# Performance work log

Measured on AMD Instinct MI355X. Metric: run time of the kernel, lower is better.

## Reference

```python
import jax, jax.numpy as jnp
import numpy as np

N = 1024  # batch


def setup_inputs() -> dict:
    key = jax.random.key(0)
    ks = jax.random.split(key, 10)
    meta_feature = jax.random.uniform(ks[0], (N, 6), dtype=jnp.float32)
    tile_wall_feature = jax.random.uniform(ks[1], (N, 34, 5), dtype=jnp.float32)
    tile_prep = jax.random.uniform(ks[2], (N, 320, 34, 7), dtype=jnp.float32)
    # keep tile_hidden_ct (channel 4) away from 0 so the division stays well-conditioned
    tile_prep = tile_prep.at[..., 4].add(0.5)
    fan_prep = jax.random.uniform(ks[3], (N, 320, 80), dtype=jnp.float32)
    redundant_tile_prep = jax.random.uniform(ks[4], (N, 320, 34), dtype=jnp.float32)
    count_prep = jax.random.uniform(ks[5], (N, 320), dtype=jnp.float32)
    chi_peng_count_remain = jax.random.uniform(ks[6], (N, 320), dtype=jnp.float32)
    # learned params: Linear(11,1) of TileProbModuleNew, fan_coeff, tile_coeff
    W_throw = jax.random.normal(ks[7], (11,), dtype=jnp.float32) * 0.05
    b_throw = jnp.array(0.5, dtype=jnp.float32)  # keeps prob_throw > 0 (faithful math; avoids NaN from neg**frac)
    fan_coeff = 0.1 + 0.015 * jax.random.normal(ks[8], (80,), dtype=jnp.float32)
    tile_coeff = 1.0 + 0.015 * jax.random.normal(ks[9], (34,), dtype=jnp.float32)
    fan_coeff_multiplier = jnp.ones((80,), dtype=jnp.float32).at[33].set(21.0)
    return {
        'meta_feature': meta_feature,
        'tile_wall_feature': tile_wall_feature,
        'tile_prep': tile_prep,
        'fan_prep': fan_prep,
        'redundant_tile_prep': redundant_tile_prep,
        'count_prep': count_prep,
        'chi_peng_count_remain': chi_peng_count_remain,
        'W_throw': W_throw,
        'b_throw': b_throw,
        'fan_coeff': fan_coeff,
        'fan_coeff_multiplier': fan_coeff_multiplier,
        'tile_coeff': tile_coeff,
    }


def reference(meta_feature, tile_wall_feature, tile_prep, fan_prep,
              redundant_tile_prep, count_prep, chi_peng_count_remain,
              W_throw, b_throw, fan_coeff, fan_coeff_multiplier, tile_coeff):
    n = meta_feature.shape[0]
    # TileProbModuleNew: per-tile Linear(11,1)
    meta_exp = jnp.broadcast_to(meta_feature[:, None, :], (n, 34, 6))
    feat = jnp.concatenate([meta_exp, tile_wall_feature], axis=-1)        # (n,34,11)
    prob_throw = feat @ W_throw + b_throw                                  # (n,34)

    tile_self_draw_baseline = tile_prep[..., 0]
    tile_need_count = tile_prep[..., 1]
    tile_cp_coeff = tile_prep[..., 2]
    tile_cp_base = tile_prep[..., 3]
    tile_hidden_ct = tile_prep[..., 4]
    tile_cp_switch = tile_prep[..., 5]
    tile_null_filler = tile_prep[..., 6]

    fan_pref = fan_prep * fan_coeff * fan_coeff_multiplier                 # (n,320,80)
    multiplied_fan_pref = jnp.sum(fan_pref, axis=-1)                       # (n,320)

    term1 = tile_self_draw_baseline * prob_throw[:, None, :] ** tile_need_count
    term2 = jnp.nan_to_num(tile_cp_base * tile_cp_coeff / tile_hidden_ct)
    terms_summed = term1 + tile_null_filler + term2 * tile_cp_switch      # (n,320,34)

    final_prob_throw = jnp.prod(terms_summed, axis=-1) * 100.0 * multiplied_fan_pref  # (n,320)

    redundant_prob = redundant_tile_prep * final_prob_throw[..., None]    # (n,320,34)
    redundant_prob = redundant_prob.reshape(n, 5, 64, 34)
    tile_bound_winrate = redundant_prob.sum(axis=2)                        # (n,5,34)

    weighted_tile_prob = (tile_bound_winrate * tile_coeff)[:, 0]           # (n,34)

    final_prob_ops = final_prob_throw.reshape(n, 5, 64).sum(axis=-1)       # (n,5)
    max_tile_prob_for_action = jnp.max(tile_bound_winrate, axis=2)         # (n,5)
    max_tile_prob_for_action = max_tile_prob_for_action.at[:, 0].set(final_prob_ops[:, 0])
    return (max_tile_prob_for_action, weighted_tile_prob)
```

## Files before the change

### kernel.cpp

```cpp
#include <hip/hip_runtime.h>
#include <math.h>

#define N_OPS 320
#define RPC 16
#define NCHUNK 4
#define F4_PER_CHUNK 952

__global__ __launch_bounds__(256) void mahjong_kernel(
    const float* __restrict__ meta,
    const float* __restrict__ wall,
    const float* __restrict__ tile_prep,
    const float* __restrict__ fan_prep,
    const float* __restrict__ redundant,
    const float* __restrict__ W_throw,
    const float* __restrict__ b_throw,
    const float* __restrict__ fan_coeff,
    const float* __restrict__ fan_mult,
    const float* __restrict__ tile_coeff,
    float* __restrict__ out_max,
    float* __restrict__ out_weighted,
    int n)
{
    const int blk  = blockIdx.x;
    const int b    = blk / 5;
    const int g    = blk % 5;
    const int tid  = threadIdx.x;
    const int wave = tid >> 6;
    const int lane = tid & 63;

    __shared__ float4 stage4[F4_PER_CHUNK];
    __shared__ float  qp_sm[RPC * 20];
    __shared__ float  prob_sm[34];
    __shared__ float  fc_sm[80];
    __shared__ float  final_sm[64];
    __shared__ float  acc_sm[4][34];

    if (tid < 34) {
        float acc = b_throw[0];
        #pragma unroll
        for (int j = 0; j < 6; ++j) acc += meta[(size_t)b * 6 + j] * W_throw[j];
        const float* w = wall + ((size_t)b * 34 + tid) * 5;
        #pragma unroll
        for (int j = 0; j < 5; ++j) acc += w[j] * W_throw[6 + j];
        prob_sm[tid] = acc;
    }
    if (tid >= 64 && tid < 144) {
        int f = tid - 64;
        fc_sm[f] = fan_coeff[f] * fan_mult[f];
    }
    __syncthreads();

    const int r = tid >> 4;
    const int p = tid & 15;
    const int tcount = (p < 2) ? 3 : 2;
    const int t0     = (p < 2) ? 3 * p : 2 * p + 2;

    const size_t rowB = (size_t)b * N_OPS + g * 64;

    for (int c = 0; c < NCHUNK; ++c) {
        const size_t row0 = rowB + c * RPC;

        const float4* src4 = (const float4*)(tile_prep + row0 * 238);
        #pragma unroll
        for (int k = 0; k < 3; ++k) stage4[tid + 256 * k] = src4[tid + 256 * k];
        if (tid < F4_PER_CHUNK - 768) stage4[tid + 768] = src4[tid + 768];

        {
            const float4* fsrc = (const float4*)(fan_prep + row0 * 80);
            float4 v = fsrc[tid];
            int f = 4 * (tid % 20);
            qp_sm[tid] = v.x * fc_sm[f]     + v.y * fc_sm[f + 1]
                       + v.z * fc_sm[f + 2] + v.w * fc_sm[f + 3];
            if (tid < RPC * 20 - 256) {
                int i = 256 + tid;
                float4 u = fsrc[i];
                int f2 = 4 * (i % 20);
                qp_sm[i] = u.x * fc_sm[f2]     + u.y * fc_sm[f2 + 1]
                         + u.z * fc_sm[f2 + 2] + u.w * fc_sm[f2 + 3];
            }
        }
        __syncthreads();

        const float* srow = (const float*)stage4 + r * 238;
        float prod = 1.0f;
        for (int ti = 0; ti < tcount; ++ti) {
            const int t = t0 + ti;
            const float* e = srow + 7 * t;
            float c0 = e[0], c1 = e[1], c2 = e[2], c3 = e[3];
            float c4 = e[4], c5 = e[5], c6 = e[6];
            prod *= c0 * exp2f(c1 * log2f(prob_sm[t])) + c6 + (c3 * c2 / c4) * c5;
        }
        const float* qr = qp_sm + r * 20;
        float qs = (p < 4) ? (qr[2 * p] + qr[2 * p + 1]) : qr[4 + p];
        #pragma unroll
        for (int sh = 1; sh < 16; sh <<= 1) {
            prod *= __shfl_xor(prod, sh);
            qs   += __shfl_xor(qs, sh);
        }
        if (p == 0) final_sm[c * RPC + r] = prod * 100.0f * qs;
        __syncthreads();
    }

    if (lane < 34) {
        const float* rr = redundant + (rowB + wave * 16) * 34;
        float acc3 = 0.0f;
        #pragma unroll
        for (int i = 0; i < 16; ++i)
            acc3 += rr[i * 34 + lane] * final_sm[wave * 16 + i];
        acc_sm[wave][lane] = acc3;
    }
    __syncthreads();

    if (wave == 0) {
        float tbw = 0.0f;
        if (lane < 34)
            tbw = acc_sm[0][lane] + acc_sm[1][lane] + acc_sm[2][lane] + acc_sm[3][lane];
        if (g == 0) {
            if (lane < 34)
                out_weighted[(size_t)b * 34 + lane] = tbw * tile_coeff[lane];
            float fs = final_sm[lane];
            #pragma unroll
            for (int sh = 1; sh < 64; sh <<= 1) fs += __shfl_xor(fs, sh);
            if (lane == 0) out_max[(size_t)b * 5] = fs;
        } else {
            float m = (lane < 34) ? tbw : -INFINITY;
            #pragma unroll
            for (int sh = 1; sh < 64; sh <<= 1) m = fmaxf(m, __shfl_xor(m, sh));
            if (lane == 0) out_max[(size_t)b * 5 + g] = m;
        }
    }
}

extern "C" void kernel_launch(void* const* d_in, const int* in_sizes, int n_in,
                              void* d_out, int out_size, void* d_ws, size_t ws_size,
                              hipStream_t stream) {
    const float* meta       = (const float*)d_in[0];
    const float* wall       = (const float*)d_in[1];
    const float* tile_prep  = (const float*)d_in[2];
    const float* fan_prep   = (const float*)d_in[3];
    const float* redundant  = (const float*)d_in[4];
    const float* W_throw    = (const float*)d_in[7];
    const float* b_throw    = (const float*)d_in[8];
    const float* fan_coeff  = (const float*)d_in[9];
    const float* fan_mult   = (const float*)d_in[10];
    const float* tile_coeff = (const float*)d_in[11];

    int n = in_sizes[0] / 6;
    float* out_max      = (float*)d_out;
    float* out_weighted = out_max + (size_t)n * 5;

    dim3 grid(n * 5), block(256);
    hipLaunchKernelGGL(mahjong_kernel, grid, block, 0, stream,
                       meta, wall, tile_prep, fan_prep, redundant,
                       W_throw, b_throw, fan_coeff, fan_mult, tile_coeff,
                       out_max, out_weighted, n);
}
```

Measured before the change: 517.6 us.

## Give each wave its own rows and prefetch the next chunk into registers

Restructures the kernel so each wave independently handles 16 rows, two at a time, with one row per 32-lane half and one tile per lane. The next chunk of tile_prep, fan_prep and redundant data is loaded into registers while the current one is computed, and the block-wide barriers inside the chunk loop go away. log2 of prob_throw is precomputed once per tile, and the redundant-weighted sum is accumulated inline instead of in a separate pass. This adds register pressure and 32-lane reductions, and the per-wave LDS staging still depends on wave-level lockstep for correctness.

```diff
diff --git a/kernel.cpp b/kernel.cpp
--- a/kernel.cpp
+++ b/kernel.cpp
@@ -2,9 +2,6 @@
 #include <math.h>
 
 #define N_OPS 320
-#define RPC 16
-#define NCHUNK 4
-#define F4_PER_CHUNK 952
 
 __global__ __launch_bounds__(256) void mahjong_kernel(
     const float* __restrict__ meta,
@@ -21,28 +18,29 @@
     float* __restrict__ out_weighted,
     int n)
 {
-    const int blk  = blockIdx.x;
-    const int b    = blk / 5;
-    const int g    = blk % 5;
-    const int tid  = threadIdx.x;
-    const int wave = tid >> 6;
-    const int lane = tid & 63;
+    const int blk = blockIdx.x;
+    const int b   = blk / 5;
+    const int g   = blk % 5;
+    const int tid = threadIdx.x;
+    const int w   = tid >> 6;
+    const int l   = tid & 63;
+    const int h   = l >> 5;
+    const int q   = l & 31;
 
-    __shared__ float4 stage4[F4_PER_CHUNK];
-    __shared__ float  qp_sm[RPC * 20];
-    __shared__ float  prob_sm[34];
+    __shared__ float4 stage[4][119];
+    __shared__ float  lp_sm[34];
     __shared__ float  fc_sm[80];
-    __shared__ float  final_sm[64];
     __shared__ float  acc_sm[4][34];
+    __shared__ float  fsum_sm[4];
 
     if (tid < 34) {
         float acc = b_throw[0];
         #pragma unroll
         for (int j = 0; j < 6; ++j) acc += meta[(size_t)b * 6 + j] * W_throw[j];
-        const float* w = wall + ((size_t)b * 34 + tid) * 5;
+        const float* wl = wall + ((size_t)b * 34 + tid) * 5;
         #pragma unroll
-        for (int j = 0; j < 5; ++j) acc += w[j] * W_throw[6 + j];
-        prob_sm[tid] = acc;
+        for (int j = 0; j < 5; ++j) acc += wl[j] * W_throw[6 + j];
+        lp_sm[tid] = log2f(acc);
     }
     if (tid >= 64 && tid < 144) {
         int f = tid - 64;
@@ -50,83 +48,87 @@
     }
     __syncthreads();
 
-    const int r = tid >> 4;
-    const int p = tid & 15;
-    const int tcount = (p < 2) ? 3 : 2;
-    const int t0     = (p < 2) ? 3 * p : 2 * p + 2;
+    const size_t rowB = (size_t)b * N_OPS + g * 64 + w * 16;
+    const float4* fan4 = (const float4*)fan_prep;
 
-    const size_t rowB = (size_t)b * N_OPS + g * 64;
+    float acc3 = 0.0f;
+    float fsum = 0.0f;
 
-    for (int c = 0; c < NCHUNK; ++c) {
-        const size_t row0 = rowB + c * RPC;
+    const float4* s4 = (const float4*)(tile_prep + rowB * 238);
+    float4 a0 = s4[l];
+    float4 a1 = (l < 55) ? s4[64 + l] : make_float4(0.f, 0.f, 0.f, 0.f);
+    float4 fv = (q < 20) ? fan4[(rowB + h) * 20 + q] : make_float4(0.f, 0.f, 0.f, 0.f);
+    float v0 = 0.f, v1 = 0.f;
+    {
+        const float* rr = redundant + rowB * 34;
+        if (l < 34) { v0 = rr[l]; v1 = rr[34 + l]; }
+    }
 
-        const float4* src4 = (const float4*)(tile_prep + row0 * 238);
+    #pragma unroll
+    for (int c = 0; c < 8; ++c) {
+        stage[w][l] = a0;
+        if (l < 55) stage[w][64 + l] = a1;
+
+        float4 na0 = make_float4(0.f, 0.f, 0.f, 0.f);
+        float4 na1 = na0, nfv = na0;
+        float nv0 = 0.f, nv1 = 0.f;
+        if (c < 7) {
+            const size_t gr = rowB + 2 * (c + 1);
+            const float4* n4 = (const float4*)(tile_prep + gr * 238);
+            na0 = n4[l];
+            if (l < 55) na1 = n4[64 + l];
+            if (q < 20) nfv = fan4[(gr + h) * 20 + q];
+            const float* rr = redundant + gr * 34;
+            if (l < 34) { nv0 = rr[l]; nv1 = rr[34 + l]; }
+        }
+
+        float qs = 0.0f;
+        if (q < 20)
+            qs = fv.x * fc_sm[4*q]   + fv.y * fc_sm[4*q+1]
+               + fv.z * fc_sm[4*q+2] + fv.w * fc_sm[4*q+3];
+
+        const float* srow = (const float*)&stage[w][0] + h * 238;
+        const float* e = srow + 7 * q;
+        float term = e[0] * exp2f(e[1] * lp_sm[q]) + e[6] + (e[3] * e[2] / e[4]) * e[5];
+        if (q < 2) {
+            const int t2 = 32 + q;
+            const float* e2 = srow + 7 * t2;
+            term *= e2[0] * exp2f(e2[1] * lp_sm[t2]) + e2[6] + (e2[3] * e2[2] / e2[4]) * e2[5];
+        }
+
         #pragma unroll
-        for (int k = 0; k < 3; ++k) stage4[tid + 256 * k] = src4[tid + 256 * k];
-        if (tid < F4_PER_CHUNK - 768) stage4[tid + 768] = src4[tid + 768];
-
-        {
-            const float4* fsrc = (const float4*)(fan_prep + row0 * 80);
-            float4 v = fsrc[tid];
-            int f = 4 * (tid % 20);
-            qp_sm[tid] = v.x * fc_sm[f]     + v.y * fc_sm[f + 1]
-                       + v.z * fc_sm[f + 2] + v.w * fc_sm[f + 3];
-            if (tid < RPC * 20 - 256) {
-                int i = 256 + tid;
-                float4 u = fsrc[i];
-                int f2 = 4 * (i % 20);
-                qp_sm[i] = u.x * fc_sm[f2]     + u.y * fc_sm[f2 + 1]
-                         + u.z * fc_sm[f2 + 2] + u.w * fc_sm[f2 + 3];
-            }
-        }
-        __syncthreads();
-
-        const float* srow = (const float*)stage4 + r * 238;
-        float prod = 1.0f;
-        for (int ti = 0; ti < tcount; ++ti) {
-            const int t = t0 + ti;
-            const float* e = srow + 7 * t;
-            float c0 = e[0], c1 = e[1], c2 = e[2], c3 = e[3];
-            float c4 = e[4], c5 = e[5], c6 = e[6];
-            prod *= c0 * exp2f(c1 * log2f(prob_sm[t])) + c6 + (c3 * c2 / c4) * c5;
-        }
-        const float* qr = qp_sm + r * 20;
-        float qs = (p < 4) ? (qr[2 * p] + qr[2 * p + 1]) : qr[4 + p];
-        #pragma unroll
-        for (int sh = 1; sh < 16; sh <<= 1) {
-            prod *= __shfl_xor(prod, sh);
+        for (int sh = 1; sh < 32; sh <<= 1) {
+            term *= __shfl_xor(term, sh);
             qs   += __shfl_xor(qs, sh);
         }
-        if (p == 0) final_sm[c * RPC + r] = prod * 100.0f * qs;
-        __syncthreads();
+        float fin  = term * 100.0f * qs;
+        float fin0 = __shfl(fin, 0);
+        float fin1 = __shfl(fin, 32);
+
+        acc3 += v0 * fin0 + v1 * fin1;
+        fsum += fin0 + fin1;
+
+        a0 = na0; a1 = na1; fv = nfv; v0 = nv0; v1 = nv1;
     }
 
-    if (lane < 34) {
-        const float* rr = redundant + (rowB + wave * 16) * 34;
-        float acc3 = 0.0f;
-        #pragma unroll
-        for (int i = 0; i < 16; ++i)
-            acc3 += rr[i * 34 + lane] * final_sm[wave * 16 + i];
-        acc_sm[wave][lane] = acc3;
-    }
+    if (l < 34) acc_sm[w][l] = acc3;
+    if (l == 0) fsum_sm[w] = fsum;
     __syncthreads();
 
-    if (wave == 0) {
+    if (w == 0) {
         float tbw = 0.0f;
-        if (lane < 34)
-            tbw = acc_sm[0][lane] + acc_sm[1][lane] + acc_sm[2][lane] + acc_sm[3][lane];
+        if (l < 34)
+            tbw = acc_sm[0][l] + acc_sm[1][l] + acc_sm[2][l] + acc_sm[3][l];
         if (g == 0) {
-            if (lane < 34)
-                out_weighted[(size_t)b * 34 + lane] = tbw * tile_coeff[lane];
-            float fs = final_sm[lane];
-            #pragma unroll
-            for (int sh = 1; sh < 64; sh <<= 1) fs += __shfl_xor(fs, sh);
-            if (lane == 0) out_max[(size_t)b * 5] = fs;
+            if (l < 34)
+                out_weighted[(size_t)b * 34 + l] = tbw * tile_coeff[l];
+            if (l == 0)
+                out_max[(size_t)b * 5] = fsum_sm[0] + fsum_sm[1] + fsum_sm[2] + fsum_sm[3];
         } else {
-            float m = (lane < 34) ? tbw : -INFINITY;
+            float m = (l < 34) ? tbw : -INFINITY;
             #pragma unroll
             for (int sh = 1; sh < 64; sh <<= 1) m = fmaxf(m, __shfl_xor(m, sh));
-            if (lane == 0) out_max[(size_t)b * 5 + g] = m;
+            if (l == 0) out_max[(size_t)b * 5 + g] = m;
         }
     }
 }
```

After: 513.2 us. No clear change (-0.9%).
